# Optimization experiments

Measured on AMD Instinct MI355X. Metric: run time of the kernel, lower is better.

Reference implementation:

```python
import jax, jax.numpy as jnp
import numpy as np

N = 131072   # number of query points
M = 8        # number of sub-models (2x2x2 ensemble grid)
H = 128      # hidden width of each sub-model MLP
GRID = np.array([2, 2, 2])  # model_grid_shape (data-dim order)


def _cell_extents():
    """Per-model [min,max] extents in x-coordinate order (x is flipped vs data dims)."""
    i = np.arange(M)
    c0 = i % GRID[0]
    c1 = (i // GRID[0]) % GRID[1]
    c2 = i // (GRID[0] * GRID[1])
    # flipped x coord j indexes grid dim j -> x-coord order is (c2, c1, c0)
    c_x = np.stack([c2, c1, c0], axis=-1).astype(np.float32)
    g_x = GRID[::-1].astype(np.float32)
    mins = -1.0 + 2.0 * c_x / g_x
    maxs = -1.0 + 2.0 * (c_x + 1.0) / g_x
    return mins.astype(np.float32), maxs.astype(np.float32)


def setup_inputs() -> dict:
    key = jax.random.key(0)
    ks = jax.random.split(key, 6)
    s = 0.1
    x = jax.random.uniform(ks[0], (N, 3), jnp.float32, -1.0, 1.0)
    W0 = jax.random.normal(ks[1], (M, 3, H), jnp.float32) * s
    b0 = jnp.zeros((M, H), jnp.float32)
    W1 = jax.random.normal(ks[2], (M, H, H), jnp.float32) * s
    b1 = jnp.zeros((M, H), jnp.float32)
    W2 = jax.random.normal(ks[3], (M, H, H), jnp.float32) * s
    b2 = jnp.zeros((M, H), jnp.float32)
    W3 = jax.random.normal(ks[4], (M, H, 1), jnp.float32) * s
    b3 = jnp.zeros((M, 1), jnp.float32)
    mins_np, maxs_np = _cell_extents()
    return {"x": x, "W0": W0, "b0": b0, "W1": W1, "b1": b1,
            "W2": W2, "b2": b2, "W3": W3, "b3": b3,
            "mins": jnp.asarray(mins_np), "maxs": jnp.asarray(maxs_np)}


def reference(x, W0, b0, W1, b1, W2, b2, W3, b3, mins, maxs):
    g = jnp.asarray(GRID, dtype=x.dtype)
    # per-point sub-model index (matches torch: flip(-1), scale by grid, linearize)
    u = (x + 1.0) / (2.0 + 1e-6)                      # [N,3] in [0,1)
    cell = (u[:, ::-1] * g).astype(jnp.int32)         # [N,3]
    idx = cell[:, 0] + cell[:, 1] * GRID[0] + cell[:, 2] * (GRID[0] * GRID[1])

    def step(y, p):
        i, w0, b0i, w1, b1i, w2, b2i, w3, b3i, mn, mx = p
        # normalize points into this model's local [-1,1]^3 box
        xn = -1.0 + 2.0 * (x - mn) / (mx - mn)        # [N,3]
        h = jax.nn.relu(xn @ w0 + b0i)                # [N,H]
        h = jax.nn.relu(h @ w1 + b1i)
        h = jax.nn.relu(h @ w2 + b2i)
        yi = h @ w3 + b3i                             # [N,1]
        y = jnp.where((idx == i)[:, None], yi, y)
        return y, None

    y0 = jnp.zeros((x.shape[0], 1), x.dtype)
    y, _ = jax.lax.scan(step, y0,
                        (jnp.arange(M), W0, b0, W1, b1, W2, b2, W3, b3, mins, maxs))
    return y
```

## Files before the change

### kernel.cpp

```cpp
#include <hip/hip_runtime.h>
#include <hip/hip_bf16.h>


#define HDIM 128
#define LDSH 136
#define TILE 64
#define NMODEL 8
#define TILES_X 272

typedef __bf16 bf16x8 __attribute__((ext_vector_type(8)));
typedef __bf16 bf16x4 __attribute__((ext_vector_type(4)));
typedef float  f32x4  __attribute__((ext_vector_type(4)));

__device__ __forceinline__ int model_of(float x0, float x1, float x2) {
  const float den = 2.000001f;
  float u0 = (x0 + 1.0f) / den;
  float u1 = (x1 + 1.0f) / den;
  float u2 = (x2 + 1.0f) / den;
  int c0 = (int)(u2 * 2.0f);
  int c1 = (int)(u1 * 2.0f);
  int c2 = (int)(u0 * 2.0f);
  return c0 + (c1 << 1) + (c2 << 2);
}

__global__ __launch_bounds__(256)
void srn_prep_scatter(const float* __restrict__ W1, const float* __restrict__ W2,
                      const float* __restrict__ x,
                      __bf16* __restrict__ Wt1, __bf16* __restrict__ Wt2,
                      int* __restrict__ cursors, int* __restrict__ perm, int N)
{
  const int b = blockIdx.x;
  const int tid = threadIdx.x;

  if (b < 64) {
    __shared__ float lds[64][65];
    const int m   = b >> 3;
    const int r2  = b & 7;
    const int mat = r2 >> 2;
    const int ti  = (r2 >> 1) & 1;
    const int tj  = r2 & 1;
    const float* src = (mat ? W2 : W1) + m * HDIM * HDIM;
    __bf16*      dst = (mat ? Wt2 : Wt1) + m * HDIM * HDIM;
    #pragma unroll
    for (int it = 0; it < 16; ++it) {
      const int rr = (tid >> 6) + it * 4, cc = tid & 63;
      lds[rr][cc] = src[(ti * 64 + rr) * HDIM + tj * 64 + cc];
    }
    __syncthreads();
    #pragma unroll
    for (int it = 0; it < 16; ++it) {
      const int nn = (tid >> 6) + it * 4, kk = tid & 63;
      dst[(tj * 64 + nn) * HDIM + ti * 64 + kk] = (__bf16)lds[kk][nn];
    }
  } else {
    __shared__ int lc[NMODEL], lb[NMODEL];
    if (tid < NMODEL) lc[tid] = 0;
    __syncthreads();
    const int base = (b - 64) * 1024;
    int ids[4], rs[4];
    #pragma unroll
    for (int it = 0; it < 4; ++it) {
      const int i = base + it * 256 + tid;
      if (i < N) {
        ids[it] = model_of(x[3*i], x[3*i+1], x[3*i+2]);
        rs[it] = atomicAdd(&lc[ids[it]], 1);
      } else ids[it] = -1;
    }
    __syncthreads();
    if (tid < NMODEL) lb[tid] = lc[tid] ? atomicAdd(&cursors[tid], lc[tid]) : 0;
    __syncthreads();
    #pragma unroll
    for (int it = 0; it < 4; ++it) {
      const int i = base + it * 256 + tid;
      if (i < N) perm[ids[it] * N + lb[ids[it]] + rs[it]] = i;
    }
  }
}

__device__ __forceinline__ void gemm_relu(const __bf16* __restrict__ hIn,
                                          __bf16* __restrict__ hOut,
                                          const __bf16* __restrict__ Wt,
                                          const float* __restrict__ bias,
                                          int wave, int l16, int quad)
{
  const int n0 = wave * 32;
  f32x4 acc[4][2] = {};
  #pragma unroll
  for (int kk = 0; kk < 4; ++kk) {
    const int kOff = kk * 32 + quad * 8;
    bf16x8 bv0 = *(const bf16x8*)(Wt + (n0 + l16) * HDIM + kOff);
    bf16x8 bv1 = *(const bf16x8*)(Wt + (n0 + 16 + l16) * HDIM + kOff);
    #pragma unroll
    for (int r = 0; r < 4; ++r) {
      bf16x8 av = *(const bf16x8*)(hIn + (r * 16 + l16) * LDSH + kOff);
      acc[r][0] = __builtin_amdgcn_mfma_f32_16x16x32_bf16(av, bv0, acc[r][0], 0, 0, 0);
      acc[r][1] = __builtin_amdgcn_mfma_f32_16x16x32_bf16(av, bv1, acc[r][1], 0, 0, 0);
    }
  }
  const float bv0 = bias[n0 + l16];
  const float bv1 = bias[n0 + 16 + l16];
  #pragma unroll
  for (int r = 0; r < 4; ++r) {
    #pragma unroll
    for (int c = 0; c < 2; ++c) {
      const int n = n0 + c * 16 + l16;
      const float bb = c ? bv1 : bv0;
      #pragma unroll
      for (int i = 0; i < 4; ++i) {
        const int row = r * 16 + quad * 4 + i;
        float v = acc[r][c][i] + bb;
        hOut[row * LDSH + n] = (__bf16)fmaxf(v, 0.0f);
      }
    }
  }
}

__global__ __launch_bounds__(256, 4)
void srn_main(const float* __restrict__ x,
              const float* __restrict__ W0, const float* __restrict__ b0,
              const float* __restrict__ b1, const float* __restrict__ b2,
              const float* __restrict__ W3, const float* __restrict__ b3,
              const float* __restrict__ mins, const float* __restrict__ maxs,
              const __bf16* __restrict__ Wt1, const __bf16* __restrict__ Wt2,
              const int* __restrict__ cursors, const int* __restrict__ perm,
              float* __restrict__ out, int N)
{
  __shared__ __align__(16) __bf16 hA[TILE * LDSH];
  __shared__ __align__(16) __bf16 hB[TILE * LDSH];
  __shared__ float xs[TILE][3];
  __shared__ int   pid[TILE];
  __shared__ float w0s[3 * HDIM];
  __shared__ float b0s[HDIM], b1s[HDIM], b2s[HDIM], w3s[HDIM];

  const int m = blockIdx.y;
  const int tid = threadIdx.x;

  if (tid < HDIM) {
    w0s[tid]          = W0[m * 3 * HDIM + tid];
    w0s[HDIM + tid]   = W0[m * 3 * HDIM + HDIM + tid];
    w0s[2*HDIM + tid] = W0[m * 3 * HDIM + 2 * HDIM + tid];
    b0s[tid] = b0[m * HDIM + tid];
    b1s[tid] = b1[m * HDIM + tid];
    b2s[tid] = b2[m * HDIM + tid];
    w3s[tid] = W3[m * HDIM + tid];
  }
  const int cnt = cursors[m];
  const int* permSeg = perm + (size_t)m * N;
  const float mn0 = mins[3*m], mn1 = mins[3*m+1], mn2 = mins[3*m+2];
  const float mx0 = maxs[3*m], mx1 = maxs[3*m+1], mx2 = maxs[3*m+2];
  const float b3v = b3[m];
  const __bf16* Wt1m = Wt1 + m * HDIM * HDIM;
  const __bf16* Wt2m = Wt2 + m * HDIM * HDIM;
  __syncthreads();

  const int lane = tid & 63;
  const int wave = tid >> 6;
  const int l16  = lane & 15;
  const int quad = lane >> 4;

  for (int tile = blockIdx.x; tile * TILE < cnt; tile += gridDim.x) {
    const int base = tile * TILE;
    const int npts = min(TILE, cnt - base);

    if (tid < TILE) {
      if (tid < npts) {
        int p = permSeg[base + tid];
        pid[tid] = p;
        xs[tid][0] = -1.0f + 2.0f * (x[3*p]     - mn0) / (mx0 - mn0);
        xs[tid][1] = -1.0f + 2.0f * (x[3*p + 1] - mn1) / (mx1 - mn1);
        xs[tid][2] = -1.0f + 2.0f * (x[3*p + 2] - mn2) / (mx2 - mn2);
      } else {
        pid[tid] = -1;
        xs[tid][0] = 0.0f; xs[tid][1] = 0.0f; xs[tid][2] = 0.0f;
      }
    }
    __syncthreads();

    {
      const int p = tid & 63;
      const int j0 = (tid >> 6) * 32;
      const float xv0 = xs[p][0], xv1 = xs[p][1], xv2 = xs[p][2];
      #pragma unroll
      for (int j = j0; j < j0 + 32; j += 4) {
        bf16x4 pk;
        #pragma unroll
        for (int u = 0; u < 4; ++u) {
          float v = b0s[j+u] + xv0 * w0s[j+u] + xv1 * w0s[HDIM + j+u] + xv2 * w0s[2*HDIM + j+u];
          pk[u] = (__bf16)fmaxf(v, 0.0f);
        }
        *(bf16x4*)(hA + p * LDSH + j) = pk;
      }
    }
    __syncthreads();

    gemm_relu(hA, hB, Wt1m, b1s, wave, l16, quad);
    __syncthreads();
    gemm_relu(hB, hA, Wt2m, b2s, wave, l16, quad);
    __syncthreads();

    {
      const int p = tid >> 2;
      const int part = tid & 3;
      float s = 0.0f;
      #pragma unroll
      for (int kk = 0; kk < 4; ++kk) {
        bf16x8 hv = *(const bf16x8*)(hA + p * LDSH + part * 32 + kk * 8);
        const float* wp = w3s + part * 32 + kk * 8;
        #pragma unroll
        for (int u = 0; u < 8; ++u) s += (float)hv[u] * wp[u];
      }
      s += __shfl_xor(s, 1);
      s += __shfl_xor(s, 2);
      if (part == 0 && p < npts) out[pid[p]] = s + b3v;
    }
    __syncthreads();
  }
}

extern "C" void kernel_launch(void* const* d_in, const int* in_sizes, int n_in,
                              void* d_out, int out_size, void* d_ws, size_t ws_size,
                              hipStream_t stream)
{
  const float* x    = (const float*)d_in[0];
  const float* W0   = (const float*)d_in[1];
  const float* b0   = (const float*)d_in[2];
  const float* W1   = (const float*)d_in[3];
  const float* b1   = (const float*)d_in[4];
  const float* W2   = (const float*)d_in[5];
  const float* b2   = (const float*)d_in[6];
  const float* W3   = (const float*)d_in[7];
  const float* b3   = (const float*)d_in[8];
  const float* mins = (const float*)d_in[9];
  const float* maxs = (const float*)d_in[10];
  float* out = (float*)d_out;
  const int N = in_sizes[0] / 3;

  char* ws = (char*)d_ws;
  int* cursors = (int*)ws;
  int* perm    = (int*)(ws + 64);
  __bf16* Wt1  = (__bf16*)(ws + 64 + (size_t)4 * N * NMODEL);
  __bf16* Wt2  = Wt1 + NMODEL * HDIM * HDIM;

  hipMemsetAsync(cursors, 0, NMODEL * sizeof(int), stream);
  const int sb = (N + 1023) >> 10;
  srn_prep_scatter<<<dim3(64 + sb), dim3(256), 0, stream>>>(W1, W2, x, Wt1, Wt2, cursors, perm, N);
  srn_main<<<dim3(TILES_X, NMODEL), dim3(256), 0, stream>>>(
      x, W0, b0, b1, b2, W3, b3, mins, maxs, Wt1, Wt2, cursors, perm, out, N);
}
```

Baseline: 111.2 us.

## Fuse prep, scatter and MLP into one cooperative persistent kernel

Replaces the memset plus the prep/scatter and main kernel launches with a single cooperative kernel. The kernel transposes the weights, counts points per model per block, takes a grid-wide prefix sum, scatters the permutation and then runs a flat tile loop across all models, with grid.sync between phases. It is meant to remove launch overhead and the load imbalance of a fixed per-model grid. In exchange it adds two grid barriers, and the weights and biases are now read from global memory rather than staged in LDS. The old kernels remain as a fallback if the cooperative launch fails.

After: 333.4 us. 3x slower.

```diff
diff --git a/kernel.cpp b/kernel.cpp
--- a/kernel.cpp
+++ b/kernel.cpp
@@ -1,12 +1,16 @@
 #include <hip/hip_runtime.h>
 #include <hip/hip_bf16.h>
+#include <hip/hip_cooperative_groups.h>
 
 
 #define HDIM 128
 #define LDSH 136
 #define TILE 64
 #define NMODEL 8
+#define MAXG 1024
 #define TILES_X 272
+
+namespace cg = cooperative_groups;
 
 typedef __bf16 bf16x8 __attribute__((ext_vector_type(8)));
 typedef __bf16 bf16x4 __attribute__((ext_vector_type(4)));
@@ -21,60 +25,6 @@
   int c1 = (int)(u1 * 2.0f);
   int c2 = (int)(u0 * 2.0f);
   return c0 + (c1 << 1) + (c2 << 2);
-}
-
-__global__ __launch_bounds__(256)
-void srn_prep_scatter(const float* __restrict__ W1, const float* __restrict__ W2,
-                      const float* __restrict__ x,
-                      __bf16* __restrict__ Wt1, __bf16* __restrict__ Wt2,
-                      int* __restrict__ cursors, int* __restrict__ perm, int N)
-{
-  const int b = blockIdx.x;
-  const int tid = threadIdx.x;
-
-  if (b < 64) {
-    __shared__ float lds[64][65];
-    const int m   = b >> 3;
-    const int r2  = b & 7;
-    const int mat = r2 >> 2;
-    const int ti  = (r2 >> 1) & 1;
-    const int tj  = r2 & 1;
-    const float* src = (mat ? W2 : W1) + m * HDIM * HDIM;
-    __bf16*      dst = (mat ? Wt2 : Wt1) + m * HDIM * HDIM;
-    #pragma unroll
-    for (int it = 0; it < 16; ++it) {
-      const int rr = (tid >> 6) + it * 4, cc = tid & 63;
-      lds[rr][cc] = src[(ti * 64 + rr) * HDIM + tj * 64 + cc];
-    }
-    __syncthreads();
-    #pragma unroll
-    for (int it = 0; it < 16; ++it) {
-      const int nn = (tid >> 6) + it * 4, kk = tid & 63;
-      dst[(tj * 64 + nn) * HDIM + ti * 64 + kk] = (__bf16)lds[kk][nn];
-    }
-  } else {
-    __shared__ int lc[NMODEL], lb[NMODEL];
-    if (tid < NMODEL) lc[tid] = 0;
-    __syncthreads();
-    const int base = (b - 64) * 1024;
-    int ids[4], rs[4];
-    #pragma unroll
-    for (int it = 0; it < 4; ++it) {
-      const int i = base + it * 256 + tid;
-      if (i < N) {
-        ids[it] = model_of(x[3*i], x[3*i+1], x[3*i+2]);
-        rs[it] = atomicAdd(&lc[ids[it]], 1);
-      } else ids[it] = -1;
-    }
-    __syncthreads();
-    if (tid < NMODEL) lb[tid] = lc[tid] ? atomicAdd(&cursors[tid], lc[tid]) : 0;
-    __syncthreads();
-    #pragma unroll
-    for (int it = 0; it < 4; ++it) {
-      const int i = base + it * 256 + tid;
-      if (i < N) perm[ids[it] * N + lb[ids[it]] + rs[it]] = i;
-    }
-  }
 }
 
 __device__ __forceinline__ void gemm_relu(const __bf16* __restrict__ hIn,
@@ -111,6 +61,231 @@
         float v = acc[r][c][i] + bb;
         hOut[row * LDSH + n] = (__bf16)fmaxf(v, 0.0f);
       }
+    }
+  }
+}
+
+__global__ __launch_bounds__(256, 4)
+void srn_fused(const float* __restrict__ x,
+               const float* __restrict__ W0, const float* __restrict__ b0,
+               const float* __restrict__ W1, const float* __restrict__ b1,
+               const float* __restrict__ W2, const float* __restrict__ b2,
+               const float* __restrict__ W3, const float* __restrict__ b3,
+               const float* __restrict__ mins, const float* __restrict__ maxs,
+               int* __restrict__ cntG, int* __restrict__ perm,
+               __bf16* __restrict__ Wt1, __bf16* __restrict__ Wt2,
+               float* __restrict__ out, int N)
+{
+  __shared__ __align__(16) __bf16 hA[TILE * LDSH];
+  __shared__ __align__(16) __bf16 hB[TILE * LDSH];
+  __shared__ float xs[TILE][3];
+  __shared__ int   pid[TILE];
+  __shared__ int lc[NMODEL];
+  __shared__ int pre_l[NMODEL], tot_l[NMODEL], gb_l[NMODEL], tstart_l[NMODEL + 1];
+
+  const int b   = blockIdx.x;
+  const int G   = gridDim.x;
+  const int tid = threadIdx.x;
+  cg::grid_group grid = cg::this_grid();
+
+  if (b < 64) {
+    float (*tp)[65] = (float(*)[65])hA;
+    const int m   = b >> 3;
+    const int r2  = b & 7;
+    const int mat = r2 >> 2;
+    const int ti  = (r2 >> 1) & 1;
+    const int tj  = r2 & 1;
+    const float* src = (mat ? W2 : W1) + m * HDIM * HDIM;
+    __bf16*      dst = (mat ? Wt2 : Wt1) + m * HDIM * HDIM;
+    #pragma unroll
+    for (int it = 0; it < 16; ++it) {
+      const int rr = (tid >> 6) + it * 4, cc = tid & 63;
+      tp[rr][cc] = src[(ti * 64 + rr) * HDIM + tj * 64 + cc];
+    }
+    __syncthreads();
+    #pragma unroll
+    for (int it = 0; it < 16; ++it) {
+      const int nn = (tid >> 6) + it * 4, kk = tid & 63;
+      dst[(tj * 64 + nn) * HDIM + ti * 64 + kk] = (__bf16)tp[kk][nn];
+    }
+  }
+  if (tid < NMODEL) lc[tid] = 0;
+  __syncthreads();
+
+  const int ppb   = (N + G - 1) / G;
+  const int start = b * ppb;
+  int myId[4], myRank[4];
+  #pragma unroll
+  for (int it = 0; it < 4; ++it) {
+    const int o  = it * 256 + tid;
+    const int pt = start + o;
+    myId[it] = -1;
+    if (o < ppb && pt < N) {
+      myId[it] = model_of(x[3*pt], x[3*pt+1], x[3*pt+2]);
+      myRank[it] = atomicAdd(&lc[myId[it]], 1);
+    }
+  }
+  __syncthreads();
+  if (tid < NMODEL) cntG[b * NMODEL + tid] = lc[tid];
+  __threadfence();
+  grid.sync();
+
+  if (tid < NMODEL) { pre_l[tid] = 0; tot_l[tid] = 0; }
+  __syncthreads();
+  {
+    const int m = tid & 7;
+    int tot = 0, pre = 0;
+    for (int b2 = tid >> 3; b2 < G; b2 += 32) {
+      const int v = cntG[b2 * NMODEL + m];
+      tot += v;
+      if (b2 < b) pre += v;
+    }
+    atomicAdd(&tot_l[m], tot);
+    atomicAdd(&pre_l[m], pre);
+  }
+  __syncthreads();
+  if (tid == 0) {
+    int run = 0, trun = 0;
+    for (int m = 0; m < NMODEL; ++m) {
+      gb_l[m] = run;      run  += tot_l[m];
+      tstart_l[m] = trun; trun += (tot_l[m] + TILE - 1) / TILE;
+    }
+    tstart_l[NMODEL] = trun;
+  }
+  __syncthreads();
+  #pragma unroll
+  for (int it = 0; it < 4; ++it)
+    if (myId[it] >= 0)
+      perm[gb_l[myId[it]] + pre_l[myId[it]] + myRank[it]] = start + it * 256 + tid;
+  __threadfence();
+  grid.sync();
+
+  const int lane = tid & 63;
+  const int wave = tid >> 6;
+  const int l16  = lane & 15;
+  const int quad = lane >> 4;
+  const int totTiles = tstart_l[NMODEL];
+
+  for (int t = b; t < totTiles; t += G) {
+    int m = 0;
+    while (m < NMODEL - 1 && t >= tstart_l[m + 1]) ++m;
+    const int lt   = t - tstart_l[m];
+    const int base = gb_l[m] + lt * TILE;
+    const int npts = min(TILE, tot_l[m] - lt * TILE);
+    const __bf16* Wt1m = Wt1 + m * HDIM * HDIM;
+    const __bf16* Wt2m = Wt2 + m * HDIM * HDIM;
+    const float* W0m = W0 + m * 3 * HDIM;
+    const float* b0m = b0 + m * HDIM;
+    const float* b1m = b1 + m * HDIM;
+    const float* b2m = b2 + m * HDIM;
+    const float* W3m = W3 + m * HDIM;
+
+    if (tid < TILE) {
+      if (tid < npts) {
+        const float mn0 = mins[3*m], mn1 = mins[3*m+1], mn2 = mins[3*m+2];
+        const float mx0 = maxs[3*m], mx1 = maxs[3*m+1], mx2 = maxs[3*m+2];
+        int p = perm[base + tid];
+        pid[tid] = p;
+        xs[tid][0] = -1.0f + 2.0f * (x[3*p]     - mn0) / (mx0 - mn0);
+        xs[tid][1] = -1.0f + 2.0f * (x[3*p + 1] - mn1) / (mx1 - mn1);
+        xs[tid][2] = -1.0f + 2.0f * (x[3*p + 2] - mn2) / (mx2 - mn2);
+      } else {
+        pid[tid] = -1;
+        xs[tid][0] = 0.0f; xs[tid][1] = 0.0f; xs[tid][2] = 0.0f;
+      }
+    }
+    __syncthreads();
+
+    {
+      const int p = tid & 63;
+      const int j0 = (tid >> 6) * 32;
+      const float xv0 = xs[p][0], xv1 = xs[p][1], xv2 = xs[p][2];
+      #pragma unroll
+      for (int j = j0; j < j0 + 32; j += 4) {
+        bf16x4 pk;
+        #pragma unroll
+        for (int u = 0; u < 4; ++u) {
+          float v = b0m[j+u] + xv0 * W0m[j+u] + xv1 * W0m[HDIM + j+u] + xv2 * W0m[2*HDIM + j+u];
+          pk[u] = (__bf16)fmaxf(v, 0.0f);
+        }
+        *(bf16x4*)(hA + p * LDSH + j) = pk;
+      }
+    }
+    __syncthreads();
+
+    gemm_relu(hA, hB, Wt1m, b1m, wave, l16, quad);
+    __syncthreads();
+    gemm_relu(hB, hA, Wt2m, b2m, wave, l16, quad);
+    __syncthreads();
+
+    {
+      const int p = tid >> 2;
+      const int part = tid & 3;
+      float s = 0.0f;
+      #pragma unroll
+      for (int kk = 0; kk < 4; ++kk) {
+        bf16x8 hv = *(const bf16x8*)(hA + p * LDSH + part * 32 + kk * 8);
+        const float* wp = W3m + part * 32 + kk * 8;
+        #pragma unroll
+        for (int u = 0; u < 8; ++u) s += (float)hv[u] * wp[u];
+      }
+      s += __shfl_xor(s, 1);
+      s += __shfl_xor(s, 2);
+      if (part == 0 && p < npts) out[pid[p]] = s + b3[m];
+    }
+    __syncthreads();
+  }
+}
+
+__global__ __launch_bounds__(256)
+void srn_prep_scatter(const float* __restrict__ W1, const float* __restrict__ W2,
+                      const float* __restrict__ x,
+                      __bf16* __restrict__ Wt1, __bf16* __restrict__ Wt2,
+                      int* __restrict__ cursors, int* __restrict__ perm, int N)
+{
+  const int b = blockIdx.x;
+  const int tid = threadIdx.x;
+  if (b < 64) {
+    __shared__ float lds[64][65];
+    const int m   = b >> 3;
+    const int r2  = b & 7;
+    const int mat = r2 >> 2;
+    const int ti  = (r2 >> 1) & 1;
+    const int tj  = r2 & 1;
+    const float* src = (mat ? W2 : W1) + m * HDIM * HDIM;
+    __bf16*      dst = (mat ? Wt2 : Wt1) + m * HDIM * HDIM;
+    #pragma unroll
+    for (int it = 0; it < 16; ++it) {
+      const int rr = (tid >> 6) + it * 4, cc = tid & 63;
+      lds[rr][cc] = src[(ti * 64 + rr) * HDIM + tj * 64 + cc];
+    }
+    __syncthreads();
+    #pragma unroll
+    for (int it = 0; it < 16; ++it) {
+      const int nn = (tid >> 6) + it * 4, kk = tid & 63;
+      dst[(tj * 64 + nn) * HDIM + ti * 64 + kk] = (__bf16)lds[kk][nn];
+    }
+  } else {
+    __shared__ int lc[NMODEL], lb[NMODEL];
+    if (tid < NMODEL) lc[tid] = 0;
+    __syncthreads();
+    const int base = (b - 64) * 1024;
+    int ids[4], rs[4];
+    #pragma unroll
+    for (int it = 0; it < 4; ++it) {
+      const int i = base + it * 256 + tid;
+      if (i < N) {
+        ids[it] = model_of(x[3*i], x[3*i+1], x[3*i+2]);
+        rs[it] = atomicAdd(&lc[ids[it]], 1);
+      } else ids[it] = -1;
+    }
+    __syncthreads();
+    if (tid < NMODEL) lb[tid] = lc[tid] ? atomicAdd(&cursors[tid], lc[tid]) : 0;
+    __syncthreads();
+    #pragma unroll
+    for (int it = 0; it < 4; ++it) {
+      const int i = base + it * 256 + tid;
+      if (i < N) perm[ids[it] * N + lb[ids[it]] + rs[it]] = i;
     }
   }
 }
@@ -129,29 +304,21 @@
   __shared__ __align__(16) __bf16 hB[TILE * LDSH];
   __shared__ float xs[TILE][3];
   __shared__ int   pid[TILE];
-  __shared__ float w0s[3 * HDIM];
-  __shared__ float b0s[HDIM], b1s[HDIM], b2s[HDIM], w3s[HDIM];
 
   const int m = blockIdx.y;
   const int tid = threadIdx.x;
-
-  if (tid < HDIM) {
-    w0s[tid]          = W0[m * 3 * HDIM + tid];
-    w0s[HDIM + tid]   = W0[m * 3 * HDIM + HDIM + tid];
-    w0s[2*HDIM + tid] = W0[m * 3 * HDIM + 2 * HDIM + tid];
-    b0s[tid] = b0[m * HDIM + tid];
-    b1s[tid] = b1[m * HDIM + tid];
-    b2s[tid] = b2[m * HDIM + tid];
-    w3s[tid] = W3[m * HDIM + tid];
-  }
   const int cnt = cursors[m];
   const int* permSeg = perm + (size_t)m * N;
   const float mn0 = mins[3*m], mn1 = mins[3*m+1], mn2 = mins[3*m+2];
   const float mx0 = maxs[3*m], mx1 = maxs[3*m+1], mx2 = maxs[3*m+2];
-  const float b3v = b3[m];
   const __bf16* Wt1m = Wt1 + m * HDIM * HDIM;
   const __bf16* Wt2m = Wt2 + m * HDIM * HDIM;
-  __syncthreads();
+  const float* W0m = W0 + m * 3 * HDIM;
+  const float* b0m = b0 + m * HDIM;
+  const float* b1m = b1 + m * HDIM;
+  const float* b2m = b2 + m * HDIM;
+  const float* W3m = W3 + m * HDIM;
+  const float b3v = b3[m];
 
   const int lane = tid & 63;
   const int wave = tid >> 6;
@@ -161,7 +328,6 @@
   for (int tile = blockIdx.x; tile * TILE < cnt; tile += gridDim.x) {
     const int base = tile * TILE;
     const int npts = min(TILE, cnt - base);
-
     if (tid < TILE) {
       if (tid < npts) {
         int p = permSeg[base + tid];
@@ -175,7 +341,6 @@
       }
     }
     __syncthreads();
-
     {
       const int p = tid & 63;
       const int j0 = (tid >> 6) * 32;
@@ -185,19 +350,17 @@
         bf16x4 pk;
         #pragma unroll
         for (int u = 0; u < 4; ++u) {
-          float v = b0s[j+u] + xv0 * w0s[j+u] + xv1 * w0s[HDIM + j+u] + xv2 * w0s[2*HDIM + j+u];
+          float v = b0m[j+u] + xv0 * W0m[j+u] + xv1 * W0m[HDIM + j+u] + xv2 * W0m[2*HDIM + j+u];
           pk[u] = (__bf16)fmaxf(v, 0.0f);
         }
         *(bf16x4*)(hA + p * LDSH + j) = pk;
       }
     }
     __syncthreads();
-
-    gemm_relu(hA, hB, Wt1m, b1s, wave, l16, quad);
-    __syncthreads();
-    gemm_relu(hB, hA, Wt2m, b2s, wave, l16, quad);
-    __syncthreads();
-
+    gemm_relu(hA, hB, Wt1m, b1m, wave, l16, quad);
+    __syncthreads();
+    gemm_relu(hB, hA, Wt2m, b2m, wave, l16, quad);
+    __syncthreads();
     {
       const int p = tid >> 2;
       const int part = tid & 3;
@@ -205,7 +368,7 @@
       #pragma unroll
       for (int kk = 0; kk < 4; ++kk) {
         bf16x8 hv = *(const bf16x8*)(hA + p * LDSH + part * 32 + kk * 8);
-        const float* wp = w3s + part * 32 + kk * 8;
+        const float* wp = W3m + part * 32 + kk * 8;
         #pragma unroll
         for (int u = 0; u < 8; ++u) s += (float)hv[u] * wp[u];
       }
@@ -233,17 +396,37 @@
   const float* mins = (const float*)d_in[9];
   const float* maxs = (const float*)d_in[10];
   float* out = (float*)d_out;
-  const int N = in_sizes[0] / 3;
+  int N = in_sizes[0] / 3;
 
   char* ws = (char*)d_ws;
+  int* cntG    = (int*)ws;
   int* cursors = (int*)ws;
-  int* perm    = (int*)(ws + 64);
-  __bf16* Wt1  = (__bf16*)(ws + 64 + (size_t)4 * N * NMODEL);
+  int* perm    = (int*)(ws + 32768);
+  __bf16* Wt1  = (__bf16*)(ws + 32768 + (size_t)4 * N * NMODEL);
   __bf16* Wt2  = Wt1 + NMODEL * HDIM * HDIM;
 
-  hipMemsetAsync(cursors, 0, NMODEL * sizeof(int), stream);
-  const int sb = (N + 1023) >> 10;
-  srn_prep_scatter<<<dim3(64 + sb), dim3(256), 0, stream>>>(W1, W2, x, Wt1, Wt2, cursors, perm, N);
-  srn_main<<<dim3(TILES_X, NMODEL), dim3(256), 0, stream>>>(
-      x, W0, b0, b1, b2, W3, b3, mins, maxs, Wt1, Wt2, cursors, perm, out, N);
-}
+  int dev = 0;  hipGetDevice(&dev);
+  int numCU = 0;
+  hipDeviceGetAttribute(&numCU, hipDeviceAttributeMultiprocessorCount, dev);
+  int occ = 0;
+  hipOccupancyMaxActiveBlocksPerMultiprocessor(&occ, (const void*)srn_fused, 256, 0);
+  int G = occ * numCU;
+  if (G > MAXG) G = MAXG;
+
+  hipError_t err = hipErrorUnknown;
+  if (G >= 256) {
+    void* args[] = { (void*)&x, (void*)&W0, (void*)&b0, (void*)&W1, (void*)&b1,
+                     (void*)&W2, (void*)&b2, (void*)&W3, (void*)&b3,
+                     (void*)&mins, (void*)&maxs, (void*)&cntG, (void*)&perm,
+                     (void*)&Wt1, (void*)&Wt2, (void*)&out, (void*)&N };
+    err = hipLaunchCooperativeKernel((const void*)srn_fused, dim3(G), dim3(256),
+                                     args, 0, stream);
+  }
+  if (err != hipSuccess) {
+    hipMemsetAsync(cursors, 0, NMODEL * sizeof(int), stream);
+    const int sb = (N + 1023) >> 10;
+    srn_prep_scatter<<<dim3(64 + sb), dim3(256), 0, stream>>>(W1, W2, x, Wt1, Wt2, cursors, perm, N);
+    srn_main<<<dim3(TILES_X, NMODEL), dim3(256), 0, stream>>>(
+        x, W0, b0, b1, b2, W3, b3, mins, maxs, Wt1, Wt2, cursors, perm, out, N);
+  }
+}
```

## Scatter pre-normalized points with ids and drop memset and LDS weight staging

Applied to the files above, without the earlier changes.

The scatter kernel now writes each point's normalized coordinates plus its original index as a packed float4 into per-model segments. The main kernel can then read one contiguous vector instead of gathering through a permutation and recomputing the normalization. The host memset is replaced by block 0 zeroing the cursors and raising a magic ready flag, which the scatter blocks spin on; scatter blocks also shrink to 512 points each. The main kernel stops staging the small per-model vectors in LDS and reads them straight from global. The ready flag is never cleared between calls, so on repeated launches scatter blocks may add to cursors before block 0 resets them, which risks a race.

Result: slower. 202.2 us (+81.9%).

```diff
diff --git a/kernel.cpp b/kernel.cpp
--- a/kernel.cpp
+++ b/kernel.cpp
@@ -7,6 +7,8 @@
 #define TILE 64
 #define NMODEL 8
 #define TILES_X 272
+#define SCAT_PPB 512
+#define RDY_MAGIC 0x5AFE5AFE
 
 typedef __bf16 bf16x8 __attribute__((ext_vector_type(8)));
 typedef __bf16 bf16x4 __attribute__((ext_vector_type(4)));
@@ -26,13 +28,19 @@
 __global__ __launch_bounds__(256)
 void srn_prep_scatter(const float* __restrict__ W1, const float* __restrict__ W2,
                       const float* __restrict__ x,
+                      const float* __restrict__ mins, const float* __restrict__ maxs,
                       __bf16* __restrict__ Wt1, __bf16* __restrict__ Wt2,
-                      int* __restrict__ cursors, int* __restrict__ perm, int N)
-{
-  const int b = blockIdx.x;
+                      int* __restrict__ cursors, f32x4* __restrict__ xn, int N)
+{
+  const int b   = blockIdx.x;
   const int tid = threadIdx.x;
 
   if (b < 64) {
+    if (b == 0) {
+      if (tid < NMODEL) atomicExch(&cursors[tid], 0);
+      __threadfence();
+      if (tid == 0) atomicExch(&cursors[NMODEL], RDY_MAGIC);
+    }
     __shared__ float lds[64][65];
     const int m   = b >> 3;
     const int r2  = b & 7;
@@ -56,23 +64,41 @@
     __shared__ int lc[NMODEL], lb[NMODEL];
     if (tid < NMODEL) lc[tid] = 0;
     __syncthreads();
-    const int base = (b - 64) * 1024;
-    int ids[4], rs[4];
-    #pragma unroll
-    for (int it = 0; it < 4; ++it) {
+    const int base = (b - 64) * SCAT_PPB;
+    int ids[2], rs[2];
+    float px[2][3];
+    #pragma unroll
+    for (int it = 0; it < 2; ++it) {
       const int i = base + it * 256 + tid;
+      ids[it] = -1;
       if (i < N) {
-        ids[it] = model_of(x[3*i], x[3*i+1], x[3*i+2]);
+        px[it][0] = x[3*i]; px[it][1] = x[3*i+1]; px[it][2] = x[3*i+2];
+        ids[it] = model_of(px[it][0], px[it][1], px[it][2]);
         rs[it] = atomicAdd(&lc[ids[it]], 1);
-      } else ids[it] = -1;
+      }
+    }
+    __syncthreads();
+    if (tid == 0) {
+      while (atomicCAS(&cursors[NMODEL], RDY_MAGIC, RDY_MAGIC) != RDY_MAGIC) {
+        __builtin_amdgcn_s_sleep(8);
+      }
     }
     __syncthreads();
     if (tid < NMODEL) lb[tid] = lc[tid] ? atomicAdd(&cursors[tid], lc[tid]) : 0;
     __syncthreads();
     #pragma unroll
-    for (int it = 0; it < 4; ++it) {
-      const int i = base + it * 256 + tid;
-      if (i < N) perm[ids[it] * N + lb[ids[it]] + rs[it]] = i;
+    for (int it = 0; it < 2; ++it) {
+      if (ids[it] >= 0) {
+        const int m = ids[it];
+        const float mn0 = mins[3*m], mn1 = mins[3*m+1], mn2 = mins[3*m+2];
+        const float mx0 = maxs[3*m], mx1 = maxs[3*m+1], mx2 = maxs[3*m+2];
+        f32x4 v;
+        v[0] = -1.0f + 2.0f * (px[it][0] - mn0) / (mx0 - mn0);
+        v[1] = -1.0f + 2.0f * (px[it][1] - mn1) / (mx1 - mn1);
+        v[2] = -1.0f + 2.0f * (px[it][2] - mn2) / (mx2 - mn2);
+        v[3] = __int_as_float(base + it * 256 + tid);
+        xn[(size_t)m * N + lb[m] + rs[it]] = v;
+      }
     }
   }
 }
@@ -116,42 +142,30 @@
 }
 
 __global__ __launch_bounds__(256, 4)
-void srn_main(const float* __restrict__ x,
-              const float* __restrict__ W0, const float* __restrict__ b0,
+void srn_main(const float* __restrict__ W0, const float* __restrict__ b0,
               const float* __restrict__ b1, const float* __restrict__ b2,
               const float* __restrict__ W3, const float* __restrict__ b3,
-              const float* __restrict__ mins, const float* __restrict__ maxs,
               const __bf16* __restrict__ Wt1, const __bf16* __restrict__ Wt2,
-              const int* __restrict__ cursors, const int* __restrict__ perm,
+              const int* __restrict__ cursors, const f32x4* __restrict__ xn,
               float* __restrict__ out, int N)
 {
   __shared__ __align__(16) __bf16 hA[TILE * LDSH];
   __shared__ __align__(16) __bf16 hB[TILE * LDSH];
   __shared__ float xs[TILE][3];
   __shared__ int   pid[TILE];
-  __shared__ float w0s[3 * HDIM];
-  __shared__ float b0s[HDIM], b1s[HDIM], b2s[HDIM], w3s[HDIM];
-
-  const int m = blockIdx.y;
+
+  const int m   = blockIdx.y;
   const int tid = threadIdx.x;
-
-  if (tid < HDIM) {
-    w0s[tid]          = W0[m * 3 * HDIM + tid];
-    w0s[HDIM + tid]   = W0[m * 3 * HDIM + HDIM + tid];
-    w0s[2*HDIM + tid] = W0[m * 3 * HDIM + 2 * HDIM + tid];
-    b0s[tid] = b0[m * HDIM + tid];
-    b1s[tid] = b1[m * HDIM + tid];
-    b2s[tid] = b2[m * HDIM + tid];
-    w3s[tid] = W3[m * HDIM + tid];
-  }
   const int cnt = cursors[m];
-  const int* permSeg = perm + (size_t)m * N;
-  const float mn0 = mins[3*m], mn1 = mins[3*m+1], mn2 = mins[3*m+2];
-  const float mx0 = maxs[3*m], mx1 = maxs[3*m+1], mx2 = maxs[3*m+2];
-  const float b3v = b3[m];
+  const f32x4* xnSeg = xn + (size_t)m * N;
   const __bf16* Wt1m = Wt1 + m * HDIM * HDIM;
   const __bf16* Wt2m = Wt2 + m * HDIM * HDIM;
-  __syncthreads();
+  const float* W0m = W0 + m * 3 * HDIM;
+  const float* b0m = b0 + m * HDIM;
+  const float* b1m = b1 + m * HDIM;
+  const float* b2m = b2 + m * HDIM;
+  const float* W3m = W3 + m * HDIM;
+  const float b3v = b3[m];
 
   const int lane = tid & 63;
   const int wave = tid >> 6;
@@ -163,12 +177,10 @@
     const int npts = min(TILE, cnt - base);
 
     if (tid < TILE) {
+      f32x4 v = xnSeg[base + tid];
       if (tid < npts) {
-        int p = permSeg[base + tid];
-        pid[tid] = p;
-        xs[tid][0] = -1.0f + 2.0f * (x[3*p]     - mn0) / (mx0 - mn0);
-        xs[tid][1] = -1.0f + 2.0f * (x[3*p + 1] - mn1) / (mx1 - mn1);
-        xs[tid][2] = -1.0f + 2.0f * (x[3*p + 2] - mn2) / (mx2 - mn2);
+        pid[tid] = __float_as_int(v[3]);
+        xs[tid][0] = v[0]; xs[tid][1] = v[1]; xs[tid][2] = v[2];
       } else {
         pid[tid] = -1;
         xs[tid][0] = 0.0f; xs[tid][1] = 0.0f; xs[tid][2] = 0.0f;
@@ -185,7 +197,7 @@
         bf16x4 pk;
         #pragma unroll
         for (int u = 0; u < 4; ++u) {
-          float v = b0s[j+u] + xv0 * w0s[j+u] + xv1 * w0s[HDIM + j+u] + xv2 * w0s[2*HDIM + j+u];
+          float v = b0m[j+u] + xv0 * W0m[j+u] + xv1 * W0m[HDIM + j+u] + xv2 * W0m[2*HDIM + j+u];
           pk[u] = (__bf16)fmaxf(v, 0.0f);
         }
         *(bf16x4*)(hA + p * LDSH + j) = pk;
@@ -193,9 +205,9 @@
     }
     __syncthreads();
 
-    gemm_relu(hA, hB, Wt1m, b1s, wave, l16, quad);
-    __syncthreads();
-    gemm_relu(hB, hA, Wt2m, b2s, wave, l16, quad);
+    gemm_relu(hA, hB, Wt1m, b1m, wave, l16, quad);
+    __syncthreads();
+    gemm_relu(hB, hA, Wt2m, b2m, wave, l16, quad);
     __syncthreads();
 
     {
@@ -205,7 +217,7 @@
       #pragma unroll
       for (int kk = 0; kk < 4; ++kk) {
         bf16x8 hv = *(const bf16x8*)(hA + p * LDSH + part * 32 + kk * 8);
-        const float* wp = w3s + part * 32 + kk * 8;
+        const float* wp = W3m + part * 32 + kk * 8;
         #pragma unroll
         for (int u = 0; u < 8; ++u) s += (float)hv[u] * wp[u];
       }
@@ -233,17 +245,17 @@
   const float* mins = (const float*)d_in[9];
   const float* maxs = (const float*)d_in[10];
   float* out = (float*)d_out;
-  const int N = in_sizes[0] / 3;
+  int N = in_sizes[0] / 3;
 
   char* ws = (char*)d_ws;
-  int* cursors = (int*)ws;
-  int* perm    = (int*)(ws + 64);
-  __bf16* Wt1  = (__bf16*)(ws + 64 + (size_t)4 * N * NMODEL);
-  __bf16* Wt2  = Wt1 + NMODEL * HDIM * HDIM;
-
-  hipMemsetAsync(cursors, 0, NMODEL * sizeof(int), stream);
-  const int sb = (N + 1023) >> 10;
-  srn_prep_scatter<<<dim3(64 + sb), dim3(256), 0, stream>>>(W1, W2, x, Wt1, Wt2, cursors, perm, N);
+  int*   cursors = (int*)ws;
+  f32x4* xn      = (f32x4*)(ws + 64);
+  __bf16* Wt1    = (__bf16*)(ws + 64 + (size_t)16 * N * NMODEL);
+  __bf16* Wt2    = Wt1 + NMODEL * HDIM * HDIM;
+
+  const int sb = (N + SCAT_PPB - 1) / SCAT_PPB;
+  srn_prep_scatter<<<dim3(64 + sb), dim3(256), 0, stream>>>(
+      W1, W2, x, mins, maxs, Wt1, Wt2, cursors, xn, N);
   srn_main<<<dim3(TILES_X, NMODEL), dim3(256), 0, stream>>>(
-      x, W0, b0, b1, b2, W3, b3, mins, maxs, Wt1, Wt2, cursors, perm, out, N);
-}
+      W0, b0, b1, b2, W3, b3, Wt1, Wt2, cursors, xn, out, N);
+}
```
